# Performance work log

Hardware: AMD Instinct MI355X
Metric: run time of the kernel (lower is better)

Reference implementation:

```python
import jax, jax.numpy as jnp
import numpy as np

NUM_EMBEDDINGS = 8192
EMBEDDING_DIM = 64
COMMITMENT_COST = 0.25


def setup_inputs() -> dict:
    key = jax.random.key(0)
    k1, k2 = jax.random.split(key)
    inputs = jax.random.normal(k1, (32, 1024, EMBEDDING_DIM), dtype=jnp.float32)
    # matches torch init: uniform(-1/K, 1/K)
    codebook = jax.random.uniform(
        k2, (NUM_EMBEDDINGS, EMBEDDING_DIM), dtype=jnp.float32,
        minval=-1.0 / NUM_EMBEDDINGS, maxval=1.0 / NUM_EMBEDDINGS)
    return {"inputs": inputs, "codebook": codebook}


def reference(inputs, codebook):
    b, n, d = inputs.shape
    x = inputs.reshape(-1, d)  # [B*N, D]
    distances = (jnp.sum(x * x, axis=1, keepdims=True)
                 + jnp.sum(codebook * codebook, axis=1)
                 - 2.0 * jnp.matmul(x, codebook.T))
    encoding_indices = jnp.argmin(distances, axis=1)  # [B*N]
    indices = encoding_indices.reshape(b, n)
    # one-hot @ codebook is just a gather
    quantized = codebook[encoding_indices].reshape(inputs.shape)
    sg = jax.lax.stop_gradient
    codebook_loss = jnp.mean((quantized - sg(inputs)) ** 2)
    commitment_loss = jnp.mean((sg(quantized) - inputs) ** 2)
    loss = codebook_loss + COMMITMENT_COST * commitment_loss
    # straight-through estimator
    quantized_st = inputs + sg(quantized - inputs)
    return quantized_st, loss, indices
```

## Files before the change

### kernel.cpp

```cpp
#include <hip/hip_runtime.h>


#define NUM_E   8192
#define DIM     64
#define KPAD    80
#define NROWS   32768
#define NELEM   2097152
#define CAP     32
#define TMARGIN 1.5e-4f
#define ROWS_PB 64
#define WAVES   8
#define NT      32
#define FLTMAX  3.402823466e+38f

using bf16x8 = __attribute__((ext_vector_type(8))) short;
using f32x16 = __attribute__((ext_vector_type(16))) float;

__device__ __forceinline__ unsigned int f2bf(float f) {
    unsigned int u = __float_as_uint(f);
    return (u + 0x7FFFu + ((u >> 16) & 1u)) >> 16;
}

__device__ __forceinline__ float np_sumsq64_f4(const float4 v[16]) {
    float r0 = __fmul_rn(v[0].x, v[0].x), r1 = __fmul_rn(v[0].y, v[0].y);
    float r2 = __fmul_rn(v[0].z, v[0].z), r3 = __fmul_rn(v[0].w, v[0].w);
    float r4 = __fmul_rn(v[1].x, v[1].x), r5 = __fmul_rn(v[1].y, v[1].y);
    float r6 = __fmul_rn(v[1].z, v[1].z), r7 = __fmul_rn(v[1].w, v[1].w);
#pragma unroll
    for (int t = 1; t < 8; ++t) {
        r0 = __fadd_rn(r0, __fmul_rn(v[2 * t].x, v[2 * t].x));
        r1 = __fadd_rn(r1, __fmul_rn(v[2 * t].y, v[2 * t].y));
        r2 = __fadd_rn(r2, __fmul_rn(v[2 * t].z, v[2 * t].z));
        r3 = __fadd_rn(r3, __fmul_rn(v[2 * t].w, v[2 * t].w));
        r4 = __fadd_rn(r4, __fmul_rn(v[2 * t + 1].x, v[2 * t + 1].x));
        r5 = __fadd_rn(r5, __fmul_rn(v[2 * t + 1].y, v[2 * t + 1].y));
        r6 = __fadd_rn(r6, __fmul_rn(v[2 * t + 1].z, v[2 * t + 1].z));
        r7 = __fadd_rn(r7, __fmul_rn(v[2 * t + 1].w, v[2 * t + 1].w));
    }
    return __fadd_rn(__fadd_rn(__fadd_rn(r0, r1), __fadd_rn(r2, r3)),
                     __fadd_rn(__fadd_rn(r4, r5), __fadd_rn(r6, r7)));
}

__global__ __launch_bounds__(256)
void vq_prep_cb(const float* __restrict__ cb, float* __restrict__ norms,
                unsigned short* __restrict__ ebuf) {
    const int row = blockIdx.x * 256 + threadIdx.x;
    float4 e[16];
    const float4* p = reinterpret_cast<const float4*>(cb + row * DIM);
#pragma unroll
    for (int c = 0; c < 16; ++c) e[c] = p[c];
    const float nrm = np_sumsq64_f4(e);
    norms[row] = nrm;
    uint2* dst = reinterpret_cast<uint2*>(ebuf + (size_t)row * KPAD);
#pragma unroll
    for (int c = 0; c < 16; ++c) {
        uint2 w;
        w.x = f2bf(e[c].x) | (f2bf(e[c].y) << 16);
        w.y = f2bf(e[c].z) | (f2bf(e[c].w) << 16);
        dst[c] = w;
    }
    unsigned int* tail = reinterpret_cast<unsigned int*>(ebuf + (size_t)row * KPAD + DIM);
    tail[0] = f2bf(-0.5f * nrm);
#pragma unroll
    for (int j = 1; j < 8; ++j) tail[j] = 0u;
}

#define TILE_MAXV(AF, RT, OUT) do {                                             \
    f32x16 acc_;                                                                \
    _Pragma("unroll") for (int i_ = 0; i_ < 16; ++i_) acc_[i_] = 0.f;           \
    _Pragma("unroll") for (int k_ = 0; k_ < 5; ++k_)                            \
        acc_ = __builtin_amdgcn_mfma_f32_32x32x16_bf16(AF[k_], bfrag[RT][k_],   \
                                                       acc_, 0, 0, 0);          \
    float m0_ = fmaxf(fmaxf(acc_[0], acc_[1]),  fmaxf(acc_[2], acc_[3]));       \
    float m1_ = fmaxf(fmaxf(acc_[4], acc_[5]),  fmaxf(acc_[6], acc_[7]));       \
    float m2_ = fmaxf(fmaxf(acc_[8], acc_[9]),  fmaxf(acc_[10], acc_[11]));     \
    float m3_ = fmaxf(fmaxf(acc_[12], acc_[13]), fmaxf(acc_[14], acc_[15]));    \
    OUT = fmaxf(fmaxf(m0_, m1_), fmaxf(m2_, m3_));                              \
} while (0)

#define TILE_GATHER(AF, RT, THR, TIDX) do {                                     \
    f32x16 acc_;                                                                \
    _Pragma("unroll") for (int i_ = 0; i_ < 16; ++i_) acc_[i_] = 0.f;           \
    _Pragma("unroll") for (int k_ = 0; k_ < 5; ++k_)                            \
        acc_ = __builtin_amdgcn_mfma_f32_32x32x16_bf16(AF[k_], bfrag[RT][k_],   \
                                                       acc_, 0, 0, 0);          \
    float m0_ = fmaxf(fmaxf(acc_[0], acc_[1]),  fmaxf(acc_[2], acc_[3]));       \
    float m1_ = fmaxf(fmaxf(acc_[4], acc_[5]),  fmaxf(acc_[6], acc_[7]));       \
    float m2_ = fmaxf(fmaxf(acc_[8], acc_[9]),  fmaxf(acc_[10], acc_[11]));     \
    float m3_ = fmaxf(fmaxf(acc_[12], acc_[13]), fmaxf(acc_[14], acc_[15]));    \
    float tm_ = fmaxf(fmaxf(m0_, m1_), fmaxf(m2_, m3_));                        \
    if (__any(tm_ >= (THR))) {                                                  \
        const int lr_ = (RT) * 32 + l31;                                        \
        _Pragma("unroll") for (int r_ = 0; r_ < 16; ++r_) {                     \
            if (acc_[r_] >= (THR)) {                                            \
                const int crow_ = (r_ & 3) + 8 * (r_ >> 2) + 4 * half;          \
                const int pos_ = atomicAdd(&scnt[lr_], 1);                      \
                if (pos_ < CAP)                                                 \
                    sslots[lr_][pos_] = candbase + (TIDX) * 32 + crow_;         \
            }                                                                   \
        }                                                                       \
    }                                                                           \
} while (0)

__global__ __launch_bounds__(512, 4)
void vq_fused_kernel(const unsigned short* __restrict__ ebuf,
                     const float* __restrict__ x, const float* __restrict__ cb,
                     const float* __restrict__ norms,
                     float* __restrict__ out_q, float* __restrict__ out_idx,
                     float* __restrict__ out_loss) {
    const int tid  = threadIdx.x;
    const int lane = tid & 63;
    const int wid  = tid >> 6;
    const int half = lane >> 5;
    const int l31  = lane & 31;
    const int rowbase  = blockIdx.x * ROWS_PB;
    const int candbase = wid * 1024;

    __shared__ float stmax[WAVES][NT / 2][ROWS_PB];
    __shared__ float sm[WAVES][ROWS_PB];
    __shared__ float sthr[ROWS_PB];
    __shared__ int   scnt[ROWS_PB];
    __shared__ unsigned int shot[WAVES];
    __shared__ int   sslots[ROWS_PB][CAP];
    __shared__ float wloss[WAVES];

    if (tid < ROWS_PB) scnt[tid] = 0;
    if (tid < WAVES)   shot[tid] = 0u;

    bf16x8 bfrag[2][5];
#pragma unroll
    for (int rt = 0; rt < 2; ++rt) {
        const float* xrow = x + (size_t)(rowbase + rt * 32 + l31) * DIM;
#pragma unroll
        for (int ks = 0; ks < 4; ++ks) {
            const float4* p = reinterpret_cast<const float4*>(xrow + ks * 16 + half * 8);
            float4 v0 = p[0], v1 = p[1];
            bf16x8 f;
            f[0] = (short)f2bf(v0.x); f[1] = (short)f2bf(v0.y);
            f[2] = (short)f2bf(v0.z); f[3] = (short)f2bf(v0.w);
            f[4] = (short)f2bf(v1.x); f[5] = (short)f2bf(v1.y);
            f[6] = (short)f2bf(v1.z); f[7] = (short)f2bf(v1.w);
            bfrag[rt][ks] = f;
        }
        bf16x8 ft;
#pragma unroll
        for (int j = 0; j < 8; ++j) ft[j] = 0;
        if (half == 0) ft[0] = (short)0x3F80;
        bfrag[rt][4] = ft;
    }

    const unsigned short* abase = ebuf + (size_t)(candbase + l31) * KPAD + half * 8;

    bf16x8 a0[5], a1[5];
#pragma unroll
    for (int ks = 0; ks < 5; ++ks)
        a0[ks] = *reinterpret_cast<const bf16x8*>(abase + ks * 16);

    for (int t = 0; t < NT; t += 2) {
        const unsigned short* ap1 = abase + (size_t)(t + 1) * 32 * KPAD;
#pragma unroll
        for (int ks = 0; ks < 5; ++ks)
            a1[ks] = *reinterpret_cast<const bf16x8*>(ap1 + ks * 16);
        float m00, m01;
        TILE_MAXV(a0, 0, m00);
        TILE_MAXV(a0, 1, m01);
        const unsigned short* ap2 = abase + (size_t)((t + 2) & (NT - 1)) * 32 * KPAD;
#pragma unroll
        for (int ks = 0; ks < 5; ++ks)
            a0[ks] = *reinterpret_cast<const bf16x8*>(ap2 + ks * 16);
        float m10, m11;
        TILE_MAXV(a1, 0, m10);
        TILE_MAXV(a1, 1, m11);
        float p0 = fmaxf(m00, m10);
        float p1 = fmaxf(m01, m11);
        p0 = fmaxf(p0, __shfl_xor(p0, 32));
        p1 = fmaxf(p1, __shfl_xor(p1, 32));
        if (half == 0) stmax[wid][t >> 1][l31]      = p0;
        else           stmax[wid][t >> 1][32 + l31] = p1;
    }
    __syncthreads();

    {
        const int w = tid >> 6, r = tid & 63;
        float m = stmax[w][0][r];
#pragma unroll
        for (int tp = 1; tp < NT / 2; ++tp) m = fmaxf(m, stmax[w][tp][r]);
        sm[w][r] = m;
    }
    __syncthreads();
    if (tid < ROWS_PB) {
        float m = sm[0][tid];
#pragma unroll
        for (int w = 1; w < WAVES; ++w) m = fmaxf(m, sm[w][tid]);
        sthr[tid] = m - TMARGIN;
    }
    __syncthreads();

    {
        const int pair = tid >> 2, sub = tid & 3;
        const int w = pair >> 4, tp = pair & 15;
        bool hot = false;
        for (int r = sub * 16; r < sub * 16 + 16; ++r)
            hot = hot || (stmax[w][tp][r] >= sthr[r]);
        if (hot) atomicOr(&shot[w], 1u << tp);
    }
    __syncthreads();

    {
        const float thr0 = sthr[l31];
        const float thr1 = sthr[32 + l31];
        unsigned int mask = shot[wid];
        while (mask) {
            const int tp = __ffs(mask) - 1;
            mask &= mask - 1;
            const int t0 = 2 * tp;
            const unsigned short* ap0 = abase + (size_t)t0 * 32 * KPAD;
            const unsigned short* ap1 = abase + (size_t)(t0 + 1) * 32 * KPAD;
#pragma unroll
            for (int ks = 0; ks < 5; ++ks) {
                a0[ks] = *reinterpret_cast<const bf16x8*>(ap0 + ks * 16);
                a1[ks] = *reinterpret_cast<const bf16x8*>(ap1 + ks * 16);
            }
            TILE_GATHER(a0, 0, thr0, t0);
            TILE_GATHER(a0, 1, thr1, t0);
            TILE_GATHER(a1, 0, thr0, t0 + 1);
            TILE_GATHER(a1, 1, thr1, t0 + 1);
        }
    }
    __syncthreads();

    float lsum = 0.f;
    for (int i = 0; i < 8; ++i) {
        const int lr = wid * 8 + i;
        const int r  = rowbase + lr;
        const int c0 = scnt[lr];
        const bool okc = (c0 <= CAP);
        const int ncand = okc ? c0 : NUM_E;
        float4 xr[16];
        const float4* xp = reinterpret_cast<const float4*>(x + (size_t)r * DIM);
#pragma unroll
        for (int c = 0; c < 16; ++c) xr[c] = xp[c];
        const float sx = np_sumsq64_f4(xr);
        float best = FLTMAX;
        int bi = 0x7FFFFFFF;
        for (int j = lane; j < ncand; j += 64) {
            const int k = okc ? sslots[lr][j] : j;
            const float4* ep4 = reinterpret_cast<const float4*>(cb + (size_t)k * DIM);
            float dot = 0.f;
#pragma unroll
            for (int c = 0; c < 16; c += 4) {
                float4 e0 = ep4[c], e1 = ep4[c + 1], e2 = ep4[c + 2], e3 = ep4[c + 3];
                dot = fmaf(xr[c].x,     e0.x, dot); dot = fmaf(xr[c].y,     e0.y, dot);
                dot = fmaf(xr[c].z,     e0.z, dot); dot = fmaf(xr[c].w,     e0.w, dot);
                dot = fmaf(xr[c + 1].x, e1.x, dot); dot = fmaf(xr[c + 1].y, e1.y, dot);
                dot = fmaf(xr[c + 1].z, e1.z, dot); dot = fmaf(xr[c + 1].w, e1.w, dot);
                dot = fmaf(xr[c + 2].x, e2.x, dot); dot = fmaf(xr[c + 2].y, e2.y, dot);
                dot = fmaf(xr[c + 2].z, e2.z, dot); dot = fmaf(xr[c + 2].w, e2.w, dot);
                dot = fmaf(xr[c + 3].x, e3.x, dot); dot = fmaf(xr[c + 3].y, e3.y, dot);
                dot = fmaf(xr[c + 3].z, e3.z, dot); dot = fmaf(xr[c + 3].w, e3.w, dot);
            }
            const float t1 = __fadd_rn(sx, norms[k]);
            const float d2 = __fadd_rn(dot, dot);
            const float sc = __fsub_rn(t1, d2);
            if (sc < best || (sc == best && k < bi)) { best = sc; bi = k; }
        }
#pragma unroll
        for (int off = 1; off < 64; off <<= 1) {
            const float s2 = __shfl_xor(best, off);
            const int   i2 = __shfl_xor(bi, off);
            if (s2 < best || (s2 == best && i2 < bi)) { best = s2; bi = i2; }
        }
        const float ed = cb[(size_t)bi * DIM + lane];
        const float xd = x[(size_t)r * DIM + lane];
        out_q[(size_t)r * DIM + lane] = ed;
        if (lane == 0) out_idx[r] = (float)bi;
        const float dd = ed - xd;
        lsum = fmaf(dd, dd, lsum);
    }
#pragma unroll
    for (int off = 1; off < 64; off <<= 1) lsum += __shfl_xor(lsum, off);
    if (lane == 0) wloss[wid] = lsum;
    __syncthreads();
    if (tid == 0) {
        float s = 0.f;
#pragma unroll
        for (int w = 0; w < WAVES; ++w) s += wloss[w];
        atomicAdd(out_loss, s * (1.25f / (float)NELEM));
    }
}

extern "C" void kernel_launch(void* const* d_in, const int* in_sizes, int n_in,
                              void* d_out, int out_size, void* d_ws, size_t ws_size,
                              hipStream_t stream) {
    const float* x  = (const float*)d_in[0];
    const float* cb = (const float*)d_in[1];

    float* out_q    = (float*)d_out;
    float* out_loss = (float*)d_out + NELEM;
    float* out_idx  = (float*)d_out + NELEM + 1;

    float* wsf   = (float*)d_ws;
    float* norms = wsf;
    unsigned short* ebuf = (unsigned short*)(norms + NUM_E);

    hipMemsetAsync(out_loss, 0, sizeof(float), stream);
    vq_prep_cb<<<NUM_E / 256, 256, 0, stream>>>(cb, norms, ebuf);
    vq_fused_kernel<<<NROWS / ROWS_PB, 512, 0, stream>>>(ebuf, x, cb, norms,
                                                         out_q, out_idx, out_loss);
}
```

Baseline: 190.3 us.

## Split codebook across two blocks per row group and merge via atomicMin epilogue

Each 64-row group is now handled by two blocks, and each block scans half the codebook (4096 entries), so the grid doubles and there is more parallelism. Launch bounds move to 8 blocks per CU. Per-row best (score, index) keys are merged with a 64-bit atomicMin into a workspace buffer. Separate epilogue and loss kernels then gather the quantized rows and reduce the loss deterministically. The hot-tile mask is now built with per-wave ballots split by row half instead of shared atomics, which drops one barrier. The cost is two extra launches, a memset of the rowbest buffer, and the threshold now being computed over only half the codebook, so a block may collect more candidates.

```diff
diff --git a/kernel.cpp b/kernel.cpp
--- a/kernel.cpp
+++ b/kernel.cpp
@@ -10,11 +10,12 @@
 #define TMARGIN 1.5e-4f
 #define ROWS_PB 64
 #define WAVES   8
-#define NT      32
+#define NT      16
 #define FLTMAX  3.402823466e+38f
 
 using bf16x8 = __attribute__((ext_vector_type(8))) short;
 using f32x16 = __attribute__((ext_vector_type(16))) float;
+typedef unsigned long long u64;
 
 __device__ __forceinline__ unsigned int f2bf(float f) {
     unsigned int u = __float_as_uint(f);
@@ -102,30 +103,26 @@
     }                                                                           \
 } while (0)
 
-__global__ __launch_bounds__(512, 4)
+__global__ __launch_bounds__(512, 8)
 void vq_fused_kernel(const unsigned short* __restrict__ ebuf,
                      const float* __restrict__ x, const float* __restrict__ cb,
                      const float* __restrict__ norms,
-                     float* __restrict__ out_q, float* __restrict__ out_idx,
-                     float* __restrict__ out_loss) {
+                     u64* __restrict__ rowbest) {
     const int tid  = threadIdx.x;
     const int lane = tid & 63;
     const int wid  = tid >> 6;
     const int half = lane >> 5;
     const int l31  = lane & 31;
-    const int rowbase  = blockIdx.x * ROWS_PB;
-    const int candbase = wid * 1024;
+    const int rowbase  = (blockIdx.x >> 1) * ROWS_PB;
+    const int candbase = (blockIdx.x & 1) * 4096 + wid * 512;
 
     __shared__ float stmax[WAVES][NT / 2][ROWS_PB];
     __shared__ float sm[WAVES][ROWS_PB];
     __shared__ float sthr[ROWS_PB];
     __shared__ int   scnt[ROWS_PB];
-    __shared__ unsigned int shot[WAVES];
     __shared__ int   sslots[ROWS_PB][CAP];
-    __shared__ float wloss[WAVES];
 
     if (tid < ROWS_PB) scnt[tid] = 0;
-    if (tid < WAVES)   shot[tid] = 0u;
 
     bf16x8 bfrag[2][5];
 #pragma unroll
@@ -196,23 +193,25 @@
     }
     __syncthreads();
 
+    unsigned int hot0 = 0, hot1 = 0;
     {
-        const int pair = tid >> 2, sub = tid & 3;
-        const int w = pair >> 4, tp = pair & 15;
-        bool hot = false;
-        for (int r = sub * 16; r < sub * 16 + 16; ++r)
-            hot = hot || (stmax[w][tp][r] >= sthr[r]);
-        if (hot) atomicOr(&shot[w], 1u << tp);
-    }
-    __syncthreads();
+        const float th = sthr[lane];
+#pragma unroll
+        for (int tp = 0; tp < NT / 2; ++tp) {
+            const u64 b = __ballot(stmax[wid][tp][lane] >= th);
+            if (b & 0xFFFFFFFFull) hot0 |= 1u << tp;
+            if (b >> 32)           hot1 |= 1u << tp;
+        }
+    }
 
     {
         const float thr0 = sthr[l31];
         const float thr1 = sthr[32 + l31];
-        unsigned int mask = shot[wid];
-        while (mask) {
-            const int tp = __ffs(mask) - 1;
-            mask &= mask - 1;
+        unsigned int mu = hot0 | hot1;
+        while (mu) {
+            const int tp = __ffs(mu) - 1;
+            const unsigned int bit = 1u << tp;
+            mu &= mu - 1;
             const int t0 = 2 * tp;
             const unsigned short* ap0 = abase + (size_t)t0 * 32 * KPAD;
             const unsigned short* ap1 = abase + (size_t)(t0 + 1) * 32 * KPAD;
@@ -221,21 +220,24 @@
                 a0[ks] = *reinterpret_cast<const bf16x8*>(ap0 + ks * 16);
                 a1[ks] = *reinterpret_cast<const bf16x8*>(ap1 + ks * 16);
             }
-            TILE_GATHER(a0, 0, thr0, t0);
-            TILE_GATHER(a0, 1, thr1, t0);
-            TILE_GATHER(a1, 0, thr0, t0 + 1);
-            TILE_GATHER(a1, 1, thr1, t0 + 1);
-        }
-    }
-    __syncthreads();
-
-    float lsum = 0.f;
+            if (hot0 & bit) {
+                TILE_GATHER(a0, 0, thr0, t0);
+                TILE_GATHER(a1, 0, thr0, t0 + 1);
+            }
+            if (hot1 & bit) {
+                TILE_GATHER(a0, 1, thr1, t0);
+                TILE_GATHER(a1, 1, thr1, t0 + 1);
+            }
+        }
+    }
+    __syncthreads();
+
     for (int i = 0; i < 8; ++i) {
         const int lr = wid * 8 + i;
         const int r  = rowbase + lr;
         const int c0 = scnt[lr];
         const bool okc = (c0 <= CAP);
-        const int ncand = okc ? c0 : NUM_E;
+        const int ncand = okc ? c0 : 4096;
         float4 xr[16];
         const float4* xp = reinterpret_cast<const float4*>(x + (size_t)r * DIM);
 #pragma unroll
@@ -244,7 +246,7 @@
         float best = FLTMAX;
         int bi = 0x7FFFFFFF;
         for (int j = lane; j < ncand; j += 64) {
-            const int k = okc ? sslots[lr][j] : j;
+            const int k = okc ? sslots[lr][j] : ((blockIdx.x & 1) * 4096 + j);
             const float4* ep4 = reinterpret_cast<const float4*>(cb + (size_t)k * DIM);
             float dot = 0.f;
 #pragma unroll
@@ -270,23 +272,56 @@
             const int   i2 = __shfl_xor(bi, off);
             if (s2 < best || (s2 == best && i2 < bi)) { best = s2; bi = i2; }
         }
-        const float ed = cb[(size_t)bi * DIM + lane];
-        const float xd = x[(size_t)r * DIM + lane];
-        out_q[(size_t)r * DIM + lane] = ed;
-        if (lane == 0) out_idx[r] = (float)bi;
-        const float dd = ed - xd;
-        lsum = fmaf(dd, dd, lsum);
-    }
-#pragma unroll
-    for (int off = 1; off < 64; off <<= 1) lsum += __shfl_xor(lsum, off);
-    if (lane == 0) wloss[wid] = lsum;
-    __syncthreads();
-    if (tid == 0) {
+        if (lane == 0) {
+            unsigned int su = __float_as_uint(best);
+            su = (su & 0x80000000u) ? ~su : (su | 0x80000000u);
+            const u64 key = ((u64)su << 32) | (unsigned int)bi;
+            atomicMin(&rowbest[r], key);
+        }
+    }
+}
+
+__global__ __launch_bounds__(512)
+void vq_epilogue_kernel(const u64* __restrict__ rowbest,
+                        const float* __restrict__ x, const float* __restrict__ cb,
+                        float* __restrict__ out_q, float* __restrict__ out_idx,
+                        float* __restrict__ block_loss) {
+    const int lane = threadIdx.x & 63;
+    const int wv   = threadIdx.x >> 6;
+    const int r    = blockIdx.x * 8 + wv;
+    const int bi   = (int)(rowbest[r] & 0xFFFFFFFFull);
+    const float ed = cb[(size_t)bi * DIM + lane];
+    const float xd = x[(size_t)r * DIM + lane];
+    out_q[(size_t)r * DIM + lane] = ed;
+    if (lane == 0) out_idx[r] = (float)bi;
+    float dd = ed - xd;
+    dd = dd * dd;
+#pragma unroll
+    for (int off = 1; off < 64; off <<= 1) dd += __shfl_xor(dd, off);
+    __shared__ float wsum[8];
+    if (lane == 0) wsum[wv] = dd;
+    __syncthreads();
+    if (threadIdx.x == 0) {
         float s = 0.f;
 #pragma unroll
-        for (int w = 0; w < WAVES; ++w) s += wloss[w];
-        atomicAdd(out_loss, s * (1.25f / (float)NELEM));
-    }
+        for (int w = 0; w < 8; ++w) s += wsum[w];
+        block_loss[blockIdx.x] = s;
+    }
+}
+
+__global__ __launch_bounds__(256)
+void vq_loss_kernel(const float* __restrict__ block_loss,
+                    float* __restrict__ out_loss) {
+    float s = 0.f;
+    for (int i = threadIdx.x; i < NROWS / 8; i += 256) s += block_loss[i];
+#pragma unroll
+    for (int off = 1; off < 64; off <<= 1) s += __shfl_xor(s, off);
+    __shared__ float wsum[4];
+    const int lane = threadIdx.x & 63, wv = threadIdx.x >> 6;
+    if (lane == 0) wsum[wv] = s;
+    __syncthreads();
+    if (threadIdx.x == 0)
+        *out_loss = ((wsum[0] + wsum[1]) + (wsum[2] + wsum[3])) * (1.25f / (float)NELEM);
 }
 
 extern "C" void kernel_launch(void* const* d_in, const int* in_sizes, int n_in,
@@ -301,10 +336,14 @@
 
     float* wsf   = (float*)d_ws;
     float* norms = wsf;
-    unsigned short* ebuf = (unsigned short*)(norms + NUM_E);
-
-    hipMemsetAsync(out_loss, 0, sizeof(float), stream);
+    float* block_loss = norms + NUM_E;
+    u64*   rowbest = (u64*)(block_loss + NROWS / 8);
+    unsigned short* ebuf = (unsigned short*)(rowbest + NROWS);
+
+    hipMemsetAsync(rowbest, 0xFF, NROWS * sizeof(u64), stream);
     vq_prep_cb<<<NUM_E / 256, 256, 0, stream>>>(cb, norms, ebuf);
-    vq_fused_kernel<<<NROWS / ROWS_PB, 512, 0, stream>>>(ebuf, x, cb, norms,
-                                                         out_q, out_idx, out_loss);
-}
+    vq_fused_kernel<<<NROWS / ROWS_PB * 2, 512, 0, stream>>>(ebuf, x, cb, norms, rowbest);
+    vq_epilogue_kernel<<<NROWS / 8, 512, 0, stream>>>(rowbest, x, cb,
+                                                      out_q, out_idx, block_loss);
+    vq_loss_kernel<<<1, 256, 0, stream>>>(block_loss, out_loss);
+}
```

Result: slower. 697.3 us (+266.5%).
